# Kernel tuning notes

Hardware: AMD Instinct MI355X
Metric: run time of the kernel (lower is better)

The kernel has to match this reference:

```python
import jax, jax.numpy as jnp
import numpy as np

GROUPS = 4
EPS = 1e-5


def _distill(x, fc1_w, fc1_b, ln_w, ln_b, fc2_w, fc2_b):
    # x: [N, cs, H, W] -> gated x (the 'input * gate' output of ChannelGate_sub)
    p = x.mean(axis=(2, 3))                     # global avg pool -> [N, cs]
    p = p @ fc1_w.T + fc1_b                     # 1x1 conv == dense on pooled vec
    mu = p.mean(axis=-1, keepdims=True)         # LayerNorm over [cs,1,1] == over channel dim
    var = jnp.mean((p - mu) ** 2, axis=-1, keepdims=True)
    p = (p - mu) * jax.lax.rsqrt(var + EPS) * ln_w + ln_b
    p = jax.nn.relu(p)
    p = p @ fc2_w.T + fc2_b
    g = jax.nn.sigmoid(p)                       # [N, cs]
    return x * g[:, :, None, None]


def _forward(x, cweight, cbias, sweight, sbias, gn_w, gn_b,
             fc1_w, fc1_b, ln_w, ln_b, fc2_w, fc2_b):
    b, c, h, w = x.shape
    x = x.reshape(b * GROUPS, c // GROUPS, h, w)
    cs = c // (2 * GROUPS)
    x0, x1 = x[:, :cs], x[:, cs:]               # chunk(2, dim=1)

    # channel-attention branch
    xn = x0.mean(axis=(2, 3), keepdims=True)    # [N, cs, 1, 1]
    xn = cweight * xn + cbias
    xn = x0 * jax.nn.sigmoid(xn)
    x_reid_0 = x0 - xn
    xn = xn + _distill(x_reid_0, fc1_w, fc1_b, ln_w, ln_b, fc2_w, fc2_b)

    # spatial-attention branch: GroupNorm(cs groups, cs channels) == per-channel instance norm
    mu = x1.mean(axis=(2, 3), keepdims=True)
    var = jnp.mean((x1 - mu) ** 2, axis=(2, 3), keepdims=True)
    xs = (x1 - mu) * jax.lax.rsqrt(var + EPS)
    xs = xs * gn_w[None, :, None, None] + gn_b[None, :, None, None]
    xs = sweight * xs + sbias
    xs = x1 * jax.nn.sigmoid(xs)
    x_reid_1 = x1 - xs
    xs = xs + _distill(x_reid_1, fc1_w, fc1_b, ln_w, ln_b, fc2_w, fc2_b)

    out = jnp.concatenate([xn, xs], axis=1)
    return out.reshape(b, c, h, w)


def setup_inputs() -> dict:
    key = jax.random.key(0)
    ks = jax.random.split(key, 14)
    B, C, H, W = 32, 256, 64, 64
    cs = C // (2 * GROUPS)  # 32
    s = 0.1
    return {
        "x": jax.random.normal(ks[0], (B, C, H, W), jnp.float32),
        "cweight": jax.random.normal(ks[1], (1, cs, 1, 1), jnp.float32) * s,
        "cbias": jnp.ones((1, cs, 1, 1), jnp.float32) + jax.random.normal(ks[2], (1, cs, 1, 1), jnp.float32) * s,
        "sweight": jax.random.normal(ks[3], (1, cs, H, W), jnp.float32) * s,
        "sbias": jnp.ones((1, cs, 1, 1), jnp.float32) + jax.random.normal(ks[4], (1, cs, 1, 1), jnp.float32) * s,
        "gn_w": jnp.ones((cs,), jnp.float32) + jax.random.normal(ks[5], (cs,), jnp.float32) * s,
        "gn_b": jax.random.normal(ks[6], (cs,), jnp.float32) * s,
        "fc1_w": jax.random.normal(ks[7], (cs, cs), jnp.float32) * (1.0 / np.sqrt(cs)),
        "fc1_b": jax.random.normal(ks[8], (cs,), jnp.float32) * s,
        "ln_w": jnp.ones((cs,), jnp.float32) + jax.random.normal(ks[9], (cs,), jnp.float32) * s,
        "ln_b": jax.random.normal(ks[10], (cs,), jnp.float32) * s,
        "fc2_w": jax.random.normal(ks[11], (cs, cs), jnp.float32) * (1.0 / np.sqrt(cs)),
        "fc2_b": jax.random.normal(ks[12], (cs,), jnp.float32) * s,
    }


def reference(x, cweight, cbias, sweight, sbias, gn_w, gn_b,
              fc1_w, fc1_b, ln_w, ln_b, fc2_w, fc2_b):
    return _forward(x, cweight, cbias, sweight, sbias, gn_w, gn_b,
                    fc1_w, fc1_b, ln_w, ln_b, fc2_w, fc2_b)
```

## Files before the change

kernel.cpp:

```cpp
#include <hip/hip_runtime.h>
#include <math.h>

#define HW 4096
#define CS 32
#define NS 128
#define NPLANES 8192
#define EPS 1e-5f

__device__ __forceinline__ float sigmoidf_(float x) {
    return 1.0f / (1.0f + __expf(-x));
}

__device__ __forceinline__ float block_reduce(float s, float* ls, int tid) {
    for (int off = 32; off > 0; off >>= 1) s += __shfl_down(s, off, 64);
    const int wave = tid >> 6, lane = tid & 63;
    if (lane == 0) ls[wave] = s;
    __syncthreads();
    return ls[0] + ls[1] + ls[2] + ls[3];
}

__global__ __launch_bounds__(256) void pass1_kernel(
    const float* __restrict__ x,
    const float* __restrict__ gnw, const float* __restrict__ gnb,
    const float* __restrict__ sw,  const float* __restrict__ sb,
    float* __restrict__ sums0, float* __restrict__ mu1,
    float* __restrict__ rs1,   float* __restrict__ sumxs) {
    const int P = blockIdx.x;
    const int n = P >> 6, cc = P & 63;
    const int tid = threadIdx.x;
    const float4* xp = (const float4*)(x + (size_t)P * HW);
    __shared__ float ls[4];
    __shared__ float bc[2];

    if (cc < CS) {
        float s = 0.f;
#pragma unroll
        for (int k = 0; k < 4; ++k) {
            float4 v = xp[tid + k * 256];
            s += v.x + v.y + v.z + v.w;
        }
        s = block_reduce(s, ls, tid);
        if (tid == 0) sums0[n * CS + cc] = s;
    } else {
        const int c = cc - CS;
        float4 v[4];
        float s = 0.f, s2 = 0.f;
#pragma unroll
        for (int k = 0; k < 4; ++k) {
            v[k] = xp[tid + k * 256];
            s  += v[k].x + v[k].y + v[k].z + v[k].w;
            s2 += v[k].x * v[k].x + v[k].y * v[k].y
                + v[k].z * v[k].z + v[k].w * v[k].w;
        }
        for (int off = 32; off > 0; off >>= 1) {
            s  += __shfl_down(s, off, 64);
            s2 += __shfl_down(s2, off, 64);
        }
        __shared__ float ls2[4];
        const int wave = tid >> 6, lane = tid & 63;
        if (lane == 0) { ls[wave] = s; ls2[wave] = s2; }
        __syncthreads();
        if (tid == 0) {
            float st  = ls[0] + ls[1] + ls[2] + ls[3];
            float s2t = ls2[0] + ls2[1] + ls2[2] + ls2[3];
            float mu  = st * (1.0f / HW);
            float var = s2t * (1.0f / HW) - mu * mu;
            float rs  = rsqrtf(var + EPS);
            mu1[n * CS + c] = mu;
            rs1[n * CS + c] = rs;
            bc[0] = mu; bc[1] = rs;
        }
        __syncthreads();
        const float mu = bc[0], rs = bc[1];
        const float a  = gnw[c] * rs;
        const float b0 = gnb[c] - mu * a;
        const float sbv = sb[c];
        const float4* wp = (const float4*)(sw + (size_t)c * HW);
        float sx = 0.f;
#pragma unroll
        for (int k = 0; k < 4; ++k) {
            float4 w = wp[tid + k * 256];
            sx += v[k].x * sigmoidf_(w.x * (v[k].x * a + b0) + sbv);
            sx += v[k].y * sigmoidf_(w.y * (v[k].y * a + b0) + sbv);
            sx += v[k].z * sigmoidf_(w.z * (v[k].z * a + b0) + sbv);
            sx += v[k].w * sigmoidf_(w.w * (v[k].w * a + b0) + sbv);
        }
        __syncthreads();
        sx = block_reduce(sx, ls, tid);
        if (tid == 0) sumxs[n * CS + c] = sx;
    }
}

__global__ __launch_bounds__(64) void gates_kernel(
    const float* __restrict__ sums0,
    const float* __restrict__ mu1, const float* __restrict__ sumxs,
    const float* __restrict__ cw,  const float* __restrict__ cb,
    const float* __restrict__ fc1w, const float* __restrict__ fc1b,
    const float* __restrict__ lnw, const float* __restrict__ lnb,
    const float* __restrict__ fc2w, const float* __restrict__ fc2b,
    float* __restrict__ s0, float* __restrict__ gd1) {
    const int n = blockIdx.x;
    const int tid = threadIdx.x;
    const int half = tid >> 5, c = tid & 31;
    __shared__ float p[2][CS], q[2][CS], r[2][CS];
    float g0 = 0.f;
    if (half == 0) {
        float mean = sums0[n * CS + c] * (1.0f / HW);
        g0 = sigmoidf_(cw[c] * mean + cb[c]);
        p[0][c] = mean * (1.0f - g0);
    } else {
        p[1][c] = mu1[n * CS + c] - sumxs[n * CS + c] * (1.0f / HW);
    }
    __syncthreads();
    float qv = fc1b[c];
    for (int j = 0; j < CS; ++j) qv += fc1w[c * CS + j] * p[half][j];
    q[half][c] = qv;
    __syncthreads();
    float mu = 0.f;
    for (int j = 0; j < CS; ++j) mu += q[half][j];
    mu *= (1.0f / CS);
    float var = 0.f;
    for (int j = 0; j < CS; ++j) { float d = q[half][j] - mu; var += d * d; }
    var *= (1.0f / CS);
    float qn = (qv - mu) * rsqrtf(var + EPS) * lnw[c] + lnb[c];
    r[half][c] = fmaxf(qn, 0.f);
    __syncthreads();
    float sv = fc2b[c];
    for (int j = 0; j < CS; ++j) sv += fc2w[c * CS + j] * r[half][j];
    float gd = sigmoidf_(sv);
    if (half == 0) s0[n * CS + c] = g0 + (1.0f - g0) * gd;
    else           gd1[n * CS + c] = gd;
}

__global__ __launch_bounds__(256) void out_kernel(
    const float* __restrict__ x, float* __restrict__ out,
    const float* __restrict__ s0,
    const float* __restrict__ mu1, const float* __restrict__ rs1,
    const float* __restrict__ gnw, const float* __restrict__ gnb,
    const float* __restrict__ sw,  const float* __restrict__ sb,
    const float* __restrict__ gd1) {
    const int P = blockIdx.x;
    const int n = P >> 6, cc = P & 63;
    const int tid = threadIdx.x;
    const float4* xp = (const float4*)(x + (size_t)P * HW);
    float4* op = (float4*)(out + (size_t)P * HW);
    if (cc < CS) {
        const float scale = s0[n * CS + cc];
#pragma unroll
        for (int k = 0; k < 4; ++k) {
            float4 v = xp[tid + k * 256];
            v.x *= scale; v.y *= scale; v.z *= scale; v.w *= scale;
            op[tid + k * 256] = v;
        }
    } else {
        const int c = cc - CS;
        const float g  = gd1[n * CS + c];
        const float mu = mu1[n * CS + c], rs = rs1[n * CS + c];
        const float a  = gnw[c] * rs;
        const float b0 = gnb[c] - mu * a;
        const float sbv = sb[c];
        const float4* wp = (const float4*)(sw + (size_t)c * HW);
#pragma unroll
        for (int k = 0; k < 4; ++k) {
            float4 v = xp[tid + k * 256];
            float4 w = wp[tid + k * 256];
            float4 o; float sg;
            sg = sigmoidf_(w.x * (v.x * a + b0) + sbv); o.x = v.x * (sg + (1.f - sg) * g);
            sg = sigmoidf_(w.y * (v.y * a + b0) + sbv); o.y = v.y * (sg + (1.f - sg) * g);
            sg = sigmoidf_(w.z * (v.z * a + b0) + sbv); o.z = v.z * (sg + (1.f - sg) * g);
            sg = sigmoidf_(w.w * (v.w * a + b0) + sbv); o.w = v.w * (sg + (1.f - sg) * g);
            op[tid + k * 256] = o;
        }
    }
}

extern "C" void kernel_launch(void* const* d_in, const int* in_sizes, int n_in,
                              void* d_out, int out_size, void* d_ws, size_t ws_size,
                              hipStream_t stream) {
    const float* x    = (const float*)d_in[0];
    const float* cw   = (const float*)d_in[1];
    const float* cb   = (const float*)d_in[2];
    const float* sw   = (const float*)d_in[3];
    const float* sb   = (const float*)d_in[4];
    const float* gnw  = (const float*)d_in[5];
    const float* gnb  = (const float*)d_in[6];
    const float* fc1w = (const float*)d_in[7];
    const float* fc1b = (const float*)d_in[8];
    const float* lnw  = (const float*)d_in[9];
    const float* lnb  = (const float*)d_in[10];
    const float* fc2w = (const float*)d_in[11];
    const float* fc2b = (const float*)d_in[12];
    float* out = (float*)d_out;
    float* ws  = (float*)d_ws;

    float* sums0 = ws;
    float* mu1   = ws + 4096;
    float* rs1   = ws + 8192;
    float* sumxs = ws + 12288;
    float* s0    = ws + 16384;
    float* gd1   = ws + 20480;

    pass1_kernel<<<NPLANES, 256, 0, stream>>>(x, gnw, gnb, sw, sb,
                                              sums0, mu1, rs1, sumxs);
    gates_kernel<<<NS, 64, 0, stream>>>(sums0, mu1, sumxs, cw, cb,
                                        fc1w, fc1b, lnw, lnb, fc2w, fc2b,
                                        s0, gd1);
    out_kernel<<<NPLANES, 256, 0, stream>>>(x, out, s0, mu1, rs1,
                                            gnw, gnb, sw, sb, gd1);
}
```

Measured before the change: 69.19 us.

## Fuse gate MLP into output kernel and use nontemporal stores

New measurement: 67.77 us. -2.0%, faster.

```diff
diff --git a/kernel.cpp b/kernel.cpp
--- a/kernel.cpp
+++ b/kernel.cpp
@@ -7,8 +7,14 @@
 #define NPLANES 8192
 #define EPS 1e-5f
 
+typedef float vfloat4 __attribute__((ext_vector_type(4)));
+
 __device__ __forceinline__ float sigmoidf_(float x) {
     return 1.0f / (1.0f + __expf(-x));
+}
+
+__device__ __forceinline__ void nt_store4(float4* p, float4 v) {
+    __builtin_nontemporal_store(*(const vfloat4*)&v, (vfloat4*)p);
 }
 
 __device__ __forceinline__ float block_reduce(float s, float* ls, int tid) {
@@ -91,75 +97,84 @@
     }
 }
 
-__global__ __launch_bounds__(64) void gates_kernel(
+__global__ __launch_bounds__(256) void out_kernel(
+    const float* __restrict__ x, float* __restrict__ out,
     const float* __restrict__ sums0,
-    const float* __restrict__ mu1, const float* __restrict__ sumxs,
+    const float* __restrict__ mu1, const float* __restrict__ rs1,
+    const float* __restrict__ sumxs,
     const float* __restrict__ cw,  const float* __restrict__ cb,
+    const float* __restrict__ gnw, const float* __restrict__ gnb,
+    const float* __restrict__ sw,  const float* __restrict__ sb,
     const float* __restrict__ fc1w, const float* __restrict__ fc1b,
     const float* __restrict__ lnw, const float* __restrict__ lnb,
-    const float* __restrict__ fc2w, const float* __restrict__ fc2b,
-    float* __restrict__ s0, float* __restrict__ gd1) {
-    const int n = blockIdx.x;
-    const int tid = threadIdx.x;
-    const int half = tid >> 5, c = tid & 31;
-    __shared__ float p[2][CS], q[2][CS], r[2][CS];
-    float g0 = 0.f;
-    if (half == 0) {
-        float mean = sums0[n * CS + c] * (1.0f / HW);
-        g0 = sigmoidf_(cw[c] * mean + cb[c]);
-        p[0][c] = mean * (1.0f - g0);
-    } else {
-        p[1][c] = mu1[n * CS + c] - sumxs[n * CS + c] * (1.0f / HW);
-    }
-    __syncthreads();
-    float qv = fc1b[c];
-    for (int j = 0; j < CS; ++j) qv += fc1w[c * CS + j] * p[half][j];
-    q[half][c] = qv;
-    __syncthreads();
-    float mu = 0.f;
-    for (int j = 0; j < CS; ++j) mu += q[half][j];
-    mu *= (1.0f / CS);
-    float var = 0.f;
-    for (int j = 0; j < CS; ++j) { float d = q[half][j] - mu; var += d * d; }
-    var *= (1.0f / CS);
-    float qn = (qv - mu) * rsqrtf(var + EPS) * lnw[c] + lnb[c];
-    r[half][c] = fmaxf(qn, 0.f);
-    __syncthreads();
-    float sv = fc2b[c];
-    for (int j = 0; j < CS; ++j) sv += fc2w[c * CS + j] * r[half][j];
-    float gd = sigmoidf_(sv);
-    if (half == 0) s0[n * CS + c] = g0 + (1.0f - g0) * gd;
-    else           gd1[n * CS + c] = gd;
-}
-
-__global__ __launch_bounds__(256) void out_kernel(
-    const float* __restrict__ x, float* __restrict__ out,
-    const float* __restrict__ s0,
-    const float* __restrict__ mu1, const float* __restrict__ rs1,
-    const float* __restrict__ gnw, const float* __restrict__ gnb,
-    const float* __restrict__ sw,  const float* __restrict__ sb,
-    const float* __restrict__ gd1) {
+    const float* __restrict__ fc2w, const float* __restrict__ fc2b) {
     const int P = blockIdx.x;
     const int n = P >> 6, cc = P & 63;
     const int tid = threadIdx.x;
+    const int branch = (cc >= CS);
+    const int c0 = cc & 31;
+
+    __shared__ float pS[CS], qS[CS], rS[CS], g0S[CS];
+    __shared__ float scaleS;
+
+    if (tid < CS) {
+        float pv;
+        if (!branch) {
+            float mean = sums0[n * CS + tid] * (1.0f / HW);
+            float g0 = sigmoidf_(cw[tid] * mean + cb[tid]);
+            g0S[tid] = g0;
+            pv = mean * (1.0f - g0);
+        } else {
+            pv = mu1[n * CS + tid] - sumxs[n * CS + tid] * (1.0f / HW);
+        }
+        pS[tid] = pv;
+    }
+    __syncthreads();
+    if (tid < CS) {
+        float qv = fc1b[tid];
+        for (int j = 0; j < CS; ++j) qv += fc1w[tid * CS + j] * pS[j];
+        qS[tid] = qv;
+    }
+    __syncthreads();
+    if (tid < CS) {
+        float mu = 0.f;
+        for (int j = 0; j < CS; ++j) mu += qS[j];
+        mu *= (1.0f / CS);
+        float var = 0.f;
+        for (int j = 0; j < CS; ++j) { float d = qS[j] - mu; var += d * d; }
+        var *= (1.0f / CS);
+        float qn = (qS[tid] - mu) * rsqrtf(var + EPS) * lnw[tid] + lnb[tid];
+        rS[tid] = fmaxf(qn, 0.f);
+    }
+    __syncthreads();
+    if (tid < 64) {
+        float t = (tid < CS) ? fc2w[c0 * CS + tid] * rS[tid] : 0.f;
+        for (int off = 32; off > 0; off >>= 1) t += __shfl_down(t, off, 64);
+        if (tid == 0) {
+            float gd = sigmoidf_(t + fc2b[c0]);
+            scaleS = branch ? gd : (g0S[c0] + (1.0f - g0S[c0]) * gd);
+        }
+    }
+    __syncthreads();
+
     const float4* xp = (const float4*)(x + (size_t)P * HW);
     float4* op = (float4*)(out + (size_t)P * HW);
-    if (cc < CS) {
-        const float scale = s0[n * CS + cc];
+
+    if (!branch) {
+        const float scale = scaleS;
 #pragma unroll
         for (int k = 0; k < 4; ++k) {
             float4 v = xp[tid + k * 256];
             v.x *= scale; v.y *= scale; v.z *= scale; v.w *= scale;
-            op[tid + k * 256] = v;
+            nt_store4(op + tid + k * 256, v);
         }
     } else {
-        const int c = cc - CS;
-        const float g  = gd1[n * CS + c];
-        const float mu = mu1[n * CS + c], rs = rs1[n * CS + c];
-        const float a  = gnw[c] * rs;
-        const float b0 = gnb[c] - mu * a;
-        const float sbv = sb[c];
-        const float4* wp = (const float4*)(sw + (size_t)c * HW);
+        const float g  = scaleS;
+        const float mu = mu1[n * CS + c0], rs = rs1[n * CS + c0];
+        const float a  = gnw[c0] * rs;
+        const float b0 = gnb[c0] - mu * a;
+        const float sbv = sb[c0];
+        const float4* wp = (const float4*)(sw + (size_t)c0 * HW);
 #pragma unroll
         for (int k = 0; k < 4; ++k) {
             float4 v = xp[tid + k * 256];
@@ -169,7 +184,7 @@
             sg = sigmoidf_(w.y * (v.y * a + b0) + sbv); o.y = v.y * (sg + (1.f - sg) * g);
             sg = sigmoidf_(w.z * (v.z * a + b0) + sbv); o.z = v.z * (sg + (1.f - sg) * g);
             sg = sigmoidf_(w.w * (v.w * a + b0) + sbv); o.w = v.w * (sg + (1.f - sg) * g);
-            op[tid + k * 256] = o;
+            nt_store4(op + tid + k * 256, o);
         }
     }
 }
@@ -197,14 +212,10 @@
     float* mu1   = ws + 4096;
     float* rs1   = ws + 8192;
     float* sumxs = ws + 12288;
-    float* s0    = ws + 16384;
-    float* gd1   = ws + 20480;
 
     pass1_kernel<<<NPLANES, 256, 0, stream>>>(x, gnw, gnb, sw, sb,
                                               sums0, mu1, rs1, sumxs);
-    gates_kernel<<<NS, 64, 0, stream>>>(sums0, mu1, sumxs, cw, cb,
-                                        fc1w, fc1b, lnw, lnb, fc2w, fc2b,
-                                        s0, gd1);
-    out_kernel<<<NPLANES, 256, 0, stream>>>(x, out, s0, mu1, rs1,
-                                            gnw, gnb, sw, sb, gd1);
-}
+    out_kernel<<<NPLANES, 256, 0, stream>>>(x, out, sums0, mu1, rs1, sumxs,
+                                            cw, cb, gnw, gnb, sw, sb,
+                                            fc1w, fc1b, lnw, lnb, fc2w, fc2b);
+}
```
